# Optimization experiments

Measured on AMD Instinct MI355X. Metric: run time of the kernel, lower is better.

## Reference

```python
import jax, jax.numpy as jnp
import numpy as np

HIDDEN = 4096
NUM_HEADS = 32
GROUP_NUM = 8
HEAD_DIM = HIDDEN // NUM_HEADS


def setup_inputs() -> dict:
    key = jax.random.key(0)
    ks = jax.random.split(key, 9)
    s = 0.02
    kv_dim = GROUP_NUM * HEAD_DIM
    return {
        "hidden_state": jax.random.normal(ks[0], (1, 2048, HIDDEN), dtype=jnp.float32),
        "wq": jax.random.normal(ks[1], (HIDDEN, HIDDEN), dtype=jnp.float32) * s,
        "bq": jnp.zeros((HIDDEN,), dtype=jnp.float32),
        "wk": jax.random.normal(ks[2], (HIDDEN, kv_dim), dtype=jnp.float32) * s,
        "bk": jnp.zeros((kv_dim,), dtype=jnp.float32),
        "wv": jax.random.normal(ks[3], (HIDDEN, kv_dim), dtype=jnp.float32) * s,
        "bv": jnp.zeros((kv_dim,), dtype=jnp.float32),
        "wo": jax.random.normal(ks[4], (HIDDEN, HIDDEN), dtype=jnp.float32) * s,
        "bo": jnp.zeros((HIDDEN,), dtype=jnp.float32),
    }


def reference(hidden_state, wq, bq, wk, bk, wv, bv, wo, bo):
    B, S, _ = hidden_state.shape
    q = hidden_state @ wq + bq                      # [B,S,H*D]
    k = hidden_state @ wk + bk                      # [B,S,G*D]
    v = hidden_state @ wv + bv                      # [B,S,G*D]

    q = q.reshape(B, S, NUM_HEADS, HEAD_DIM).transpose(0, 2, 1, 3)   # [B,H,S,D]
    k = k.reshape(B, S, GROUP_NUM, HEAD_DIM).transpose(0, 2, 1, 3)   # [B,G,S,D]
    v = v.reshape(B, S, GROUP_NUM, HEAD_DIM).transpose(0, 2, 1, 3)
    # broadcast KV groups to all heads (repeat each group heads_per_group times)
    rep = NUM_HEADS // GROUP_NUM
    k = jnp.repeat(k, rep, axis=1)                  # [B,H,S,D]
    v = jnp.repeat(v, rep, axis=1)

    scale = 1.0 / jnp.sqrt(jnp.float32(HEAD_DIM))
    scores = jnp.einsum("bhqd,bhkd->bhqk", q, k) * scale  # [B,H,S,S]
    probs = jax.nn.softmax(scores, axis=-1)
    out = jnp.einsum("bhqk,bhkd->bhqd", probs, v)         # [B,H,S,D]
    # faithful to original: transpose(-1,-2) then view (NOT a standard head merge)
    out = jnp.swapaxes(out, -1, -2).reshape(B, -1, HEAD_DIM * NUM_HEADS)  # [B,S,H*D]
    return out @ wo + bo
```

## Files before the change

### kernel.cpp

```cpp
#include <hip/hip_runtime.h>
#include <stdint.h>

#define HIDDEN 4096
#define SEQ    2048
#define NHEADS 32
#define HDIM   128
#define KVDIM  1024

typedef __attribute__((ext_vector_type(8))) short short8;
typedef __attribute__((ext_vector_type(4))) unsigned short ushort4v;
typedef __attribute__((ext_vector_type(4))) float f32x4;
typedef __attribute__((ext_vector_type(16))) float f32x16;
typedef __attribute__((ext_vector_type(4))) float float4v;
typedef __attribute__((ext_vector_type(4))) int int4v;

__device__ __forceinline__ unsigned short f2bf(float f) {
    union { float f; unsigned u; } v; v.f = f;
    unsigned r = v.u + 0x7FFFu + ((v.u >> 16) & 1u);
    return (unsigned short)(r >> 16);
}

__device__ __forceinline__ float fexp2(float x) {
#if __has_builtin(__builtin_amdgcn_exp2f)
    return __builtin_amdgcn_exp2f(x);
#else
    return exp2f(x);
#endif
}

__device__ __forceinline__ void store_elem(unsigned short* p, float v) { *p = f2bf(v); }
__device__ __forceinline__ void store_elem(float* p, float v) { *p = v; }

__global__ void cast_bf16_kernel(const float* __restrict__ in,
                                 unsigned short* __restrict__ out, int n4) {
    int i = blockIdx.x * blockDim.x + threadIdx.x;
    if (i >= n4) return;
    float4v v = *(const float4v*)(in + (size_t)i * 4);
    ushort4v o;
    o.x = f2bf(v.x); o.y = f2bf(v.y); o.z = f2bf(v.z); o.w = f2bf(v.w);
    *(ushort4v*)(out + (size_t)i * 4) = o;
}

__global__ void transpose_cast_all_kernel(const float* __restrict__ wq,
                                          const float* __restrict__ wk,
                                          const float* __restrict__ wv,
                                          const float* __restrict__ wo,
                                          unsigned short* __restrict__ wqkvt,
                                          unsigned short* __restrict__ wot) {
    __shared__ float tile[64][65];
    int cx = blockIdx.x;
    const float* src; unsigned short* dst; int C; int cxl;
    if (cx < 64)      { src = wq; dst = wqkvt; C = HIDDEN; cxl = cx; }
    else if (cx < 80) { src = wk; dst = wqkvt + (size_t)4096 * HIDDEN; C = KVDIM; cxl = cx - 64; }
    else if (cx < 96) { src = wv; dst = wqkvt + (size_t)5120 * HIDDEN; C = KVDIM; cxl = cx - 80; }
    else              { src = wo; dst = wot;   C = HIDDEN; cxl = cx - 96; }
    const int R = HIDDEN;
    int r0 = blockIdx.y << 6, c0 = cxl << 6;
    int t = threadIdx.x;
    int lr = t >> 4, lc = (t & 15) << 2;
#pragma unroll
    for (int i = 0; i < 4; i++) {
        int r = lr + i * 16;
        float4v v = *(const float4v*)(src + (size_t)(r0 + r) * C + c0 + lc);
        tile[r][lc] = v.x; tile[r][lc + 1] = v.y;
        tile[r][lc + 2] = v.z; tile[r][lc + 3] = v.w;
    }
    __syncthreads();
#pragma unroll
    for (int i = 0; i < 4; i++) {
        int c = lr + i * 16;
        ushort4v o;
        o.x = f2bf(tile[lc][c]);     o.y = f2bf(tile[lc + 1][c]);
        o.z = f2bf(tile[lc + 2][c]); o.w = f2bf(tile[lc + 3][c]);
        *(ushort4v*)(dst + (size_t)(c0 + c) * R + r0 + lc) = o;
    }
}

__device__ __forceinline__ void gload_lds16(const void* g, void* l) {
    __builtin_amdgcn_global_load_lds(
        (const __attribute__((address_space(1))) void*)g,
        (__attribute__((address_space(3))) void*)l, 16, 0, 0);
}

template <typename OT>
__global__ __launch_bounds__(256, 2)
void gemm_bf16_kernel(const unsigned short* __restrict__ A,
                      const unsigned short* __restrict__ Bt,
                      const float* __restrict__ bias,
                      OT* __restrict__ C,
                      int M, int N, int K, float oscale) {
    __shared__ __align__(16) unsigned short As[128 * 32];
    __shared__ __align__(16) unsigned short Bs[128 * 32];
    int t = threadIdx.x;
    int w = t >> 6, l = t & 63;
    int wr = w >> 1, wc = w & 1;
    int fr = l & 15, fq = l >> 4;
    int mbase = blockIdx.y << 7, nbase = blockIdx.x << 7;

    const unsigned short* Ap = A + (size_t)(mbase + w * 16 + (l >> 2)) * K + ((l & 3) << 3);
    const unsigned short* Bp = Bt + (size_t)(nbase + w * 16 + (l >> 2)) * K + ((l & 3) << 3);
    unsigned short* AsW = As + w * 512;
    unsigned short* BsW = Bs + w * 512;
    const size_t rowK64 = (size_t)64 * K;

    f32x4 acc[4][4];
    f32x4 z = {0.f, 0.f, 0.f, 0.f};
#pragma unroll
    for (int m = 0; m < 4; m++)
#pragma unroll
        for (int n = 0; n < 4; n++) acc[m][n] = z;

    for (int kb = 0; kb < K; kb += 32) {
        __syncthreads();
        gload_lds16(Ap + kb,          AsW);
        gload_lds16(Ap + kb + rowK64, AsW + 2048);
        gload_lds16(Bp + kb,          BsW);
        gload_lds16(Bp + kb + rowK64, BsW + 2048);
        __syncthreads();
        short8 a[4], b[4];
#pragma unroll
        for (int m = 0; m < 4; m++)
            a[m] = *(const short8*)(As + ((wr * 64 + m * 16 + fr) * 32 + fq * 8));
#pragma unroll
        for (int n = 0; n < 4; n++)
            b[n] = *(const short8*)(Bs + ((wc * 64 + n * 16 + fr) * 32 + fq * 8));
#pragma unroll
        for (int m = 0; m < 4; m++)
#pragma unroll
            for (int n = 0; n < 4; n++)
                acc[m][n] = __builtin_amdgcn_mfma_f32_16x16x32_bf16(a[m], b[n], acc[m][n], 0, 0, 0);
    }

#pragma unroll
    for (int n = 0; n < 4; n++) {
        int col = nbase + wc * 64 + n * 16 + fr;
        float bv = bias[col];
#pragma unroll
        for (int m = 0; m < 4; m++) {
            int row = mbase + wr * 64 + m * 16 + fq * 4;
            OT* cp = C + (size_t)row * N + col;
#pragma unroll
            for (int r = 0; r < 4; r++)
                store_elem(cp + (size_t)r * N, (acc[m][n][r] + bv) * oscale);
        }
    }
}

__global__ __launch_bounds__(256, 2)
void qkv_gemm_kernel(const unsigned short* __restrict__ A,
                     const unsigned short* __restrict__ Bt,
                     const float* __restrict__ bq,
                     const float* __restrict__ bk,
                     const float* __restrict__ bv,
                     unsigned short* __restrict__ Qo,
                     unsigned short* __restrict__ Ko,
                     unsigned short* __restrict__ Vto,
                     float qscale) {
    const int K = HIDDEN;
    __shared__ __align__(16) unsigned short As[128 * 32];
    __shared__ __align__(16) unsigned short Bs[128 * 32];
    int t = threadIdx.x;
    int w = t >> 6, l = t & 63;
    int wr = w >> 1, wc = w & 1;
    int fr = l & 15, fq = l >> 4;
    int mbase = blockIdx.y << 7, nbase = blockIdx.x << 7;

    const unsigned short* Ap = A + (size_t)(mbase + w * 16 + (l >> 2)) * K + ((l & 3) << 3);
    const unsigned short* Bp = Bt + (size_t)(nbase + w * 16 + (l >> 2)) * K + ((l & 3) << 3);
    unsigned short* AsW = As + w * 512;
    unsigned short* BsW = Bs + w * 512;
    const size_t rowK64 = (size_t)64 * K;

    f32x4 acc[4][4];
    f32x4 z = {0.f, 0.f, 0.f, 0.f};
#pragma unroll
    for (int m = 0; m < 4; m++)
#pragma unroll
        for (int n = 0; n < 4; n++) acc[m][n] = z;

    for (int kb = 0; kb < K; kb += 32) {
        __syncthreads();
        gload_lds16(Ap + kb,          AsW);
        gload_lds16(Ap + kb + rowK64, AsW + 2048);
        gload_lds16(Bp + kb,          BsW);
        gload_lds16(Bp + kb + rowK64, BsW + 2048);
        __syncthreads();
        short8 a[4], b[4];
#pragma unroll
        for (int m = 0; m < 4; m++)
            a[m] = *(const short8*)(As + ((wr * 64 + m * 16 + fr) * 32 + fq * 8));
#pragma unroll
        for (int n = 0; n < 4; n++)
            b[n] = *(const short8*)(Bs + ((wc * 64 + n * 16 + fr) * 32 + fq * 8));
#pragma unroll
        for (int m = 0; m < 4; m++)
#pragma unroll
            for (int n = 0; n < 4; n++)
                acc[m][n] = __builtin_amdgcn_mfma_f32_16x16x32_bf16(a[m], b[n], acc[m][n], 0, 0, 0);
    }

    if (nbase < 4096) {
#pragma unroll
        for (int n = 0; n < 4; n++) {
            int col = nbase + wc * 64 + n * 16 + fr;
            float bb = bq[col];
#pragma unroll
            for (int m = 0; m < 4; m++) {
                int row = mbase + wr * 64 + m * 16 + fq * 4;
                unsigned short* cp = Qo + (size_t)row * HIDDEN + col;
#pragma unroll
                for (int r = 0; r < 4; r++)
                    cp[(size_t)r * HIDDEN] = f2bf((acc[m][n][r] + bb) * qscale);
            }
        }
    } else if (nbase < 5120) {
#pragma unroll
        for (int n = 0; n < 4; n++) {
            int col = nbase - 4096 + wc * 64 + n * 16 + fr;
            float bb = bk[col];
#pragma unroll
            for (int m = 0; m < 4; m++) {
                int row = mbase + wr * 64 + m * 16 + fq * 4;
                unsigned short* cp = Ko + (size_t)row * KVDIM + col;
#pragma unroll
                for (int r = 0; r < 4; r++)
                    cp[(size_t)r * KVDIM] = f2bf(acc[m][n][r] + bb);
            }
        }
    } else {
#pragma unroll
        for (int n = 0; n < 4; n++) {
            int colv = nbase - 5120 + wc * 64 + n * 16 + fr;
            float bb = bv[colv];
#pragma unroll
            for (int m = 0; m < 4; m++) {
                int row = mbase + wr * 64 + m * 16 + fq * 4;
                ushort4v o;
                o.x = f2bf(acc[m][n][0] + bb);
                o.y = f2bf(acc[m][n][1] + bb);
                o.z = f2bf(acc[m][n][2] + bb);
                o.w = f2bf(acc[m][n][3] + bb);
                *(ushort4v*)(Vto + (size_t)colv * SEQ + row) = o;
            }
        }
    }
}

#define SWZ(off, row) ((off) ^ (((row) & 7) << 4))
__global__ __launch_bounds__(256, 2)
void attn_kernel(const unsigned short* __restrict__ Q,
                 const unsigned short* __restrict__ Kc,
                 const unsigned short* __restrict__ Vt,
                 unsigned short* __restrict__ Mg) {
    __shared__ __align__(16) char Kb[2][64 * 256];
    __shared__ __align__(16) char Vb[2][128 * 128];
    int qb = blockIdx.x, head = blockIdx.y, g = head >> 2;
    int t = threadIdx.x, w = t >> 6, l = t & 63;
    int lq = l & 31, lh = l >> 5;

    short8 qf[8];
    {
        const unsigned short* qp =
            Q + (size_t)(qb * 128 + w * 32 + lq) * HIDDEN + head * HDIM + lh * 8;
#pragma unroll
        for (int kk = 0; kk < 8; kk++) qf[kk] = *(const short8*)(qp + kk * 16);
    }

    f32x16 accO[4];
#pragma unroll
    for (int n = 0; n < 4; n++)
#pragma unroll
        for (int r = 0; r < 16; r++) accO[n][r] = 0.f;
    float Lrun = 0.f;

    int krow = t >> 2; int kcb = (t & 3) * 64;
    int vrow = t >> 1; int vcb = (t & 1) * 64;
    const unsigned short* ksrc = Kc + (size_t)krow * KVDIM + g * HDIM + (t & 3) * 32;
    const unsigned short* vsrc = Vt + (size_t)(g * HDIM + vrow) * SEQ + (t & 1) * 32;
    int kwb = krow * 256 + kcb;
    int vwb = vrow * 128 + vcb;

    const int NT = SEQ / 64;
    short8 kreg[4], vreg[4];
#pragma unroll
    for (int j = 0; j < 4; j++) kreg[j] = *(const short8*)(ksrc + j * 8);
#pragma unroll
    for (int j = 0; j < 4; j++) vreg[j] = *(const short8*)(vsrc + j * 8);
#pragma unroll
    for (int j = 0; j < 4; j++) *(short8*)(Kb[0] + SWZ(kwb + j * 16, krow)) = kreg[j];
#pragma unroll
    for (int j = 0; j < 4; j++) *(short8*)(Vb[0] + SWZ(vwb + j * 16, vrow)) = vreg[j];
#pragma unroll
    for (int j = 0; j < 4; j++) kreg[j] = *(const short8*)(ksrc + (size_t)64 * KVDIM + j * 8);
#pragma unroll
    for (int j = 0; j < 4; j++) vreg[j] = *(const short8*)(vsrc + 64 + j * 8);

    for (int tl = 0; tl < NT; tl++) {
        int b = tl & 1;
        __syncthreads();
        if (tl + 1 < NT) {
#pragma unroll
            for (int j = 0; j < 4; j++) *(short8*)(Kb[b ^ 1] + SWZ(kwb + j * 16, krow)) = kreg[j];
#pragma unroll
            for (int j = 0; j < 4; j++) *(short8*)(Vb[b ^ 1] + SWZ(vwb + j * 16, vrow)) = vreg[j];
            if (tl + 2 < NT) {
                const unsigned short* ks = ksrc + (size_t)(tl + 2) * 64 * KVDIM;
                const unsigned short* vs = vsrc + (tl + 2) * 64;
#pragma unroll
                for (int j = 0; j < 4; j++) kreg[j] = *(const short8*)(ks + j * 8);
#pragma unroll
                for (int j = 0; j < 4; j++) vreg[j] = *(const short8*)(vs + j * 8);
            }
        }
        const char* kb = Kb[b];
        const char* vb = Vb[b];

        f32x16 s0, s1;
#pragma unroll
        for (int r = 0; r < 16; r++) { s0[r] = 0.f; s1[r] = 0.f; }
#pragma unroll
        for (int kk = 0; kk < 8; kk++) {
            int cb = kk * 32 + lh * 16;
            short8 kf0 = *(const short8*)(kb + SWZ(lq * 256 + cb, lq));
            short8 kf1 = *(const short8*)(kb + SWZ((lq + 32) * 256 + cb, lq));
            s0 = __builtin_amdgcn_mfma_f32_32x32x16_bf16(kf0, qf[kk], s0, 0, 0, 0);
            s1 = __builtin_amdgcn_mfma_f32_32x32x16_bf16(kf1, qf[kk], s1, 0, 0, 0);
        }

        float sum = 0.f;
#pragma unroll
        for (int r = 0; r < 16; r++) { s0[r] = fexp2(s0[r]); sum += s0[r]; }
#pragma unroll
        for (int r = 0; r < 16; r++) { s1[r] = fexp2(s1[r]); sum += s1[r]; }
        sum += __shfl_xor(sum, 32);
        Lrun += sum;

        int W0[8], W1[8];
#pragma unroll
        for (int i = 0; i < 8; i++)
            W0[i] = (int)((unsigned)f2bf(s0[2 * i]) | ((unsigned)f2bf(s0[2 * i + 1]) << 16));
#pragma unroll
        for (int i = 0; i < 8; i++)
            W1[i] = (int)((unsigned)f2bf(s1[2 * i]) | ((unsigned)f2bf(s1[2 * i + 1]) << 16));

        short8 pa[4];
#pragma unroll
        for (int kkp = 0; kkp < 4; kkp++) {
            int k4 = (kkp & 1) * 4;
            int o0 = (kkp < 2) ? W0[k4 + 0] : W1[k4 + 0];
            int o1 = (kkp < 2) ? W0[k4 + 1] : W1[k4 + 1];
            int o2 = (kkp < 2) ? W0[k4 + 2] : W1[k4 + 2];
            int o3 = (kkp < 2) ? W0[k4 + 3] : W1[k4 + 3];
            int Za = lh ? o0 : o2;
            int Zb = lh ? o1 : o3;
            int Xa = __shfl_xor(Za, 32);
            int Xb = __shfl_xor(Zb, 32);
            int4v pw;
            pw.x = lh ? Xa : o0;
            pw.y = lh ? Xb : o1;
            pw.z = lh ? o2 : Xa;
            pw.w = lh ? o3 : Xb;
            pa[kkp] = *(short8*)&pw;
        }

#pragma unroll
        for (int n = 0; n < 4; n++) {
            int row = n * 32 + lq;
#pragma unroll
            for (int kkp = 0; kkp < 4; kkp++) {
                short8 vf = *(const short8*)(vb + SWZ(row * 128 + kkp * 32 + lh * 16, lq));
                accO[n] = __builtin_amdgcn_mfma_f32_32x32x16_bf16(pa[kkp], vf, accO[n], 0, 0, 0);
            }
        }
    }

    float rl[16];
#pragma unroll
    for (int r = 0; r < 16; r++)
        rl[r] = 1.0f / __shfl(Lrun, (r & 3) + 8 * (r >> 2) + 4 * lh);
#pragma unroll
    for (int n = 0; n < 4; n++) {
        int d = n * 32 + lq;
        int mrow = head * 64 + (d >> 1);
#pragma unroll
        for (int g2 = 0; g2 < 4; g2++) {
            int mcol = (d & 1) * SEQ + qb * 128 + w * 32 + 8 * g2 + 4 * lh;
            ushort4v o;
            o.x = f2bf(accO[n][g2 * 4 + 0] * rl[g2 * 4 + 0]);
            o.y = f2bf(accO[n][g2 * 4 + 1] * rl[g2 * 4 + 1]);
            o.z = f2bf(accO[n][g2 * 4 + 2] * rl[g2 * 4 + 2]);
            o.w = f2bf(accO[n][g2 * 4 + 3] * rl[g2 * 4 + 3]);
            *(ushort4v*)(Mg + (size_t)mrow * HIDDEN + mcol) = o;
        }
    }
}

extern "C" void kernel_launch(void* const* d_in, const int* in_sizes, int n_in,
                              void* d_out, int out_size, void* d_ws, size_t ws_size,
                              hipStream_t stream) {
    const float* x  = (const float*)d_in[0];
    const float* wq = (const float*)d_in[1];
    const float* bq = (const float*)d_in[2];
    const float* wk = (const float*)d_in[3];
    const float* bk = (const float*)d_in[4];
    const float* wv = (const float*)d_in[5];
    const float* bv = (const float*)d_in[6];
    const float* wo = (const float*)d_in[7];
    const float* bo = (const float*)d_in[8];

    char* base = (char*)d_ws;
    unsigned short* xb     = (unsigned short*)(base + 0);
    unsigned short* wqkvt  = (unsigned short*)(base + 16777216);
    unsigned short* wot    = (unsigned short*)(base + 67108864);
    unsigned short* qbuf   = (unsigned short*)(base + 100663296);
    unsigned short* kbuf   = (unsigned short*)(base + 117440512);
    unsigned short* vtbuf  = (unsigned short*)(base + 121634816);
    unsigned short* merged = (unsigned short*)(base + 125829120);

    const float QSCALE = 0.08838834764831845f * 1.4426950408889634f;

    cast_bf16_kernel<<<(SEQ * HIDDEN / 4 + 255) / 256, 256, 0, stream>>>(x, xb, SEQ * HIDDEN / 4);
    transpose_cast_all_kernel<<<dim3(160, 64), 256, 0, stream>>>(wq, wk, wv, wo, wqkvt, wot);
    qkv_gemm_kernel<<<dim3(6144 / 128, SEQ / 128), 256, 0, stream>>>(
        xb, wqkvt, bq, bk, bv, qbuf, kbuf, vtbuf, QSCALE);
    attn_kernel<<<dim3(SEQ / 128, NHEADS), 256, 0, stream>>>(qbuf, kbuf, vtbuf, merged);
    gemm_bf16_kernel<<<dim3(HIDDEN / 128, SEQ / 128), 256, 0, stream>>>(
        merged, wot, bo, (float*)d_out, SEQ, HIDDEN, HIDDEN, 1.0f);
}
```

Measured before the change: 341.9 us.

## Rewrite GEMMs with 128x256 tiles, triple-buffered async LDS pipeline and swizzles

Replaces the two 128x128, 256-thread GEMM kernels with one templated 512-thread kernel. It uses a 128x256 tile with BK=64 and a three-stage LDS ring fed by global_load_lds, with vmcnt waits so loads for tile t+2 overlap compute. It also XOR-swizzles LDS to avoid bank conflicts, remaps workgroups across XCDs for better L2 locality, and raises MFMA priority with setprio. The cost is 144KB of LDS per block and one block per CU, so occupancy drops and latency hiding relies on the pipeline.

```diff
diff --git a/kernel.cpp b/kernel.cpp
--- a/kernel.cpp
+++ b/kernel.cpp
@@ -27,9 +27,6 @@
     return exp2f(x);
 #endif
 }
-
-__device__ __forceinline__ void store_elem(unsigned short* p, float v) { *p = f2bf(v); }
-__device__ __forceinline__ void store_elem(float* p, float v) { *p = v; }
 
 __global__ void cast_bf16_kernel(const float* __restrict__ in,
                                  unsigned short* __restrict__ out, int n4) {
@@ -82,26 +79,58 @@
         (__attribute__((address_space(3))) void*)l, 16, 0, 0);
 }
 
-template <typename OT>
-__global__ __launch_bounds__(256, 2)
-void gemm_bf16_kernel(const unsigned short* __restrict__ A,
-                      const unsigned short* __restrict__ Bt,
-                      const float* __restrict__ bias,
-                      OT* __restrict__ C,
-                      int M, int N, int K, float oscale) {
-    __shared__ __align__(16) unsigned short As[128 * 32];
-    __shared__ __align__(16) unsigned short Bs[128 * 32];
+template <int MODE>
+__global__ __launch_bounds__(512, 1)
+void gemm8_kernel(const unsigned short* __restrict__ A,
+                  const unsigned short* __restrict__ Bt,
+                  const float* __restrict__ b0,
+                  const float* __restrict__ b1,
+                  const float* __restrict__ b2,
+                  unsigned short* __restrict__ Qo,
+                  unsigned short* __restrict__ Ko,
+                  unsigned short* __restrict__ Vto,
+                  float* __restrict__ Of,
+                  float qscale) {
+    const int K = HIDDEN;
+    __shared__ __align__(16) char lds[3 * 49152];
+
     int t = threadIdx.x;
     int w = t >> 6, l = t & 63;
-    int wr = w >> 1, wc = w & 1;
     int fr = l & 15, fq = l >> 4;
-    int mbase = blockIdx.y << 7, nbase = blockIdx.x << 7;
-
-    const unsigned short* Ap = A + (size_t)(mbase + w * 16 + (l >> 2)) * K + ((l & 3) << 3);
-    const unsigned short* Bp = Bt + (size_t)(nbase + w * 16 + (l >> 2)) * K + ((l & 3) << 3);
-    unsigned short* AsW = As + w * 512;
-    unsigned short* BsW = Bs + w * 512;
-    const size_t rowK64 = (size_t)64 * K;
+    int wm = w >> 2, wn = w & 3;
+
+    int nwg = gridDim.x * gridDim.y;
+    int orig = blockIdx.y * gridDim.x + blockIdx.x;
+    int cpx = nwg >> 3;
+    int swz = (orig & 7) * cpx + (orig >> 3);
+    int bx = swz % gridDim.x, by = swz / gridDim.x;
+    int mbase = by * 128, nbase = bx * 256;
+
+    int rA = t >> 3;
+    int lch = (t & 7) ^ (rA & 7);
+    const unsigned short* pA0 = A + (size_t)(mbase + rA) * K + lch * 8;
+    const unsigned short* pA1 = pA0 + (size_t)64 * K;
+    const unsigned short* pB0 = Bt + (size_t)(nbase + rA) * K + lch * 8;
+    const unsigned short* pB1 = pB0 + (size_t)64 * K;
+    const unsigned short* pB2 = pB0 + (size_t)128 * K;
+    const unsigned short* pB3 = pB0 + (size_t)192 * K;
+    int wo16 = w * 1024;
+
+    int offA[4][2], offB[4][2];
+#pragma unroll
+    for (int m = 0; m < 4; m++) {
+        int row = wm * 64 + m * 16 + fr;
+#pragma unroll
+        for (int kk = 0; kk < 2; kk++)
+            offA[m][kk] = row * 128 + (((kk << 2) + fq) ^ (row & 7)) * 16;
+    }
+#pragma unroll
+    for (int n = 0; n < 4; n++) {
+        int row = wn * 64 + n * 16 + fr;
+#pragma unroll
+        for (int kk = 0; kk < 2; kk++)
+            offB[n][kk] = 16384 + row * 128 + (((kk << 2) + fq) ^ (row & 7)) * 16;
+    }
 
     f32x4 acc[4][4];
     f32x4 z = {0.f, 0.f, 0.f, 0.f};
@@ -110,137 +139,111 @@
 #pragma unroll
         for (int n = 0; n < 4; n++) acc[m][n] = z;
 
-    for (int kb = 0; kb < K; kb += 32) {
-        __syncthreads();
-        gload_lds16(Ap + kb,          AsW);
-        gload_lds16(Ap + kb + rowK64, AsW + 2048);
-        gload_lds16(Bp + kb,          BsW);
-        gload_lds16(Bp + kb + rowK64, BsW + 2048);
-        __syncthreads();
-        short8 a[4], b[4];
-#pragma unroll
-        for (int m = 0; m < 4; m++)
-            a[m] = *(const short8*)(As + ((wr * 64 + m * 16 + fr) * 32 + fq * 8));
-#pragma unroll
-        for (int n = 0; n < 4; n++)
-            b[n] = *(const short8*)(Bs + ((wc * 64 + n * 16 + fr) * 32 + fq * 8));
-#pragma unroll
-        for (int m = 0; m < 4; m++)
-#pragma unroll
-            for (int n = 0; n < 4; n++)
-                acc[m][n] = __builtin_amdgcn_mfma_f32_16x16x32_bf16(a[m], b[n], acc[m][n], 0, 0, 0);
-    }
-
-#pragma unroll
-    for (int n = 0; n < 4; n++) {
-        int col = nbase + wc * 64 + n * 16 + fr;
-        float bv = bias[col];
-#pragma unroll
-        for (int m = 0; m < 4; m++) {
-            int row = mbase + wr * 64 + m * 16 + fq * 4;
-            OT* cp = C + (size_t)row * N + col;
-#pragma unroll
-            for (int r = 0; r < 4; r++)
-                store_elem(cp + (size_t)r * N, (acc[m][n][r] + bv) * oscale);
-        }
-    }
-}
-
-__global__ __launch_bounds__(256, 2)
-void qkv_gemm_kernel(const unsigned short* __restrict__ A,
-                     const unsigned short* __restrict__ Bt,
-                     const float* __restrict__ bq,
-                     const float* __restrict__ bk,
-                     const float* __restrict__ bv,
-                     unsigned short* __restrict__ Qo,
-                     unsigned short* __restrict__ Ko,
-                     unsigned short* __restrict__ Vto,
-                     float qscale) {
-    const int K = HIDDEN;
-    __shared__ __align__(16) unsigned short As[128 * 32];
-    __shared__ __align__(16) unsigned short Bs[128 * 32];
-    int t = threadIdx.x;
-    int w = t >> 6, l = t & 63;
-    int wr = w >> 1, wc = w & 1;
-    int fr = l & 15, fq = l >> 4;
-    int mbase = blockIdx.y << 7, nbase = blockIdx.x << 7;
-
-    const unsigned short* Ap = A + (size_t)(mbase + w * 16 + (l >> 2)) * K + ((l & 3) << 3);
-    const unsigned short* Bp = Bt + (size_t)(nbase + w * 16 + (l >> 2)) * K + ((l & 3) << 3);
-    unsigned short* AsW = As + w * 512;
-    unsigned short* BsW = Bs + w * 512;
-    const size_t rowK64 = (size_t)64 * K;
-
-    f32x4 acc[4][4];
-    f32x4 z = {0.f, 0.f, 0.f, 0.f};
-#pragma unroll
-    for (int m = 0; m < 4; m++)
-#pragma unroll
-        for (int n = 0; n < 4; n++) acc[m][n] = z;
-
-    for (int kb = 0; kb < K; kb += 32) {
-        __syncthreads();
-        gload_lds16(Ap + kb,          AsW);
-        gload_lds16(Ap + kb + rowK64, AsW + 2048);
-        gload_lds16(Bp + kb,          BsW);
-        gload_lds16(Bp + kb + rowK64, BsW + 2048);
-        __syncthreads();
-        short8 a[4], b[4];
-#pragma unroll
-        for (int m = 0; m < 4; m++)
-            a[m] = *(const short8*)(As + ((wr * 64 + m * 16 + fr) * 32 + fq * 8));
-#pragma unroll
-        for (int n = 0; n < 4; n++)
-            b[n] = *(const short8*)(Bs + ((wc * 64 + n * 16 + fr) * 32 + fq * 8));
-#pragma unroll
-        for (int m = 0; m < 4; m++)
-#pragma unroll
-            for (int n = 0; n < 4; n++)
-                acc[m][n] = __builtin_amdgcn_mfma_f32_16x16x32_bf16(a[m], b[n], acc[m][n], 0, 0, 0);
-    }
-
-    if (nbase < 4096) {
+    const int NT = K / 64;
+
+#define STAGE6(bufbase, ts)                                            \
+    {                                                                  \
+        size_t ko = (size_t)(ts) * 64;                                 \
+        char* lb = lds + (bufbase);                                    \
+        gload_lds16(pA0 + ko, lb + wo16);                              \
+        gload_lds16(pA1 + ko, lb + 8192 + wo16);                       \
+        gload_lds16(pB0 + ko, lb + 16384 + wo16);                      \
+        gload_lds16(pB1 + ko, lb + 24576 + wo16);                      \
+        gload_lds16(pB2 + ko, lb + 32768 + wo16);                      \
+        gload_lds16(pB3 + ko, lb + 40960 + wo16);                      \
+    }
+
+    STAGE6(0, 0);
+    STAGE6(49152, 1);
+
+    int cb = 0;
+    for (int tt = 0; tt < NT; ++tt) {
+        if (tt + 1 < NT) asm volatile("s_waitcnt vmcnt(6)" ::: "memory");
+        else             asm volatile("s_waitcnt vmcnt(0)" ::: "memory");
+        __builtin_amdgcn_s_barrier();
+        __builtin_amdgcn_sched_barrier(0);
+        if (tt + 2 < NT) {
+            int sb = (cb == 0) ? 2 : cb - 1;
+            STAGE6(sb * 49152, tt + 2);
+        }
+        const char* base = lds + cb * 49152;
+#pragma unroll
+        for (int kk = 0; kk < 2; kk++) {
+            short8 af[4], bf[4];
+#pragma unroll
+            for (int m = 0; m < 4; m++) af[m] = *(const short8*)(base + offA[m][kk]);
+#pragma unroll
+            for (int n = 0; n < 4; n++) bf[n] = *(const short8*)(base + offB[n][kk]);
+            __builtin_amdgcn_s_setprio(1);
+#pragma unroll
+            for (int m = 0; m < 4; m++)
+#pragma unroll
+                for (int n = 0; n < 4; n++)
+                    acc[m][n] = __builtin_amdgcn_mfma_f32_16x16x32_bf16(af[m], bf[n], acc[m][n], 0, 0, 0);
+            __builtin_amdgcn_s_setprio(0);
+        }
+        cb = (cb == 2) ? 0 : cb + 1;
+    }
+#undef STAGE6
+
+    if (MODE == 1) {
+        if (nbase < 4096) {
+#pragma unroll
+            for (int n = 0; n < 4; n++) {
+                int col = nbase + wn * 64 + n * 16 + fr;
+                float bb = b0[col];
+#pragma unroll
+                for (int m = 0; m < 4; m++) {
+                    int row = mbase + wm * 64 + m * 16 + fq * 4;
+                    unsigned short* cp = Qo + (size_t)row * HIDDEN + col;
+#pragma unroll
+                    for (int r = 0; r < 4; r++)
+                        cp[(size_t)r * HIDDEN] = f2bf((acc[m][n][r] + bb) * qscale);
+                }
+            }
+        } else if (nbase < 5120) {
+#pragma unroll
+            for (int n = 0; n < 4; n++) {
+                int col = nbase - 4096 + wn * 64 + n * 16 + fr;
+                float bb = b1[col];
+#pragma unroll
+                for (int m = 0; m < 4; m++) {
+                    int row = mbase + wm * 64 + m * 16 + fq * 4;
+                    unsigned short* cp = Ko + (size_t)row * KVDIM + col;
+#pragma unroll
+                    for (int r = 0; r < 4; r++)
+                        cp[(size_t)r * KVDIM] = f2bf(acc[m][n][r] + bb);
+                }
+            }
+        } else {
+#pragma unroll
+            for (int n = 0; n < 4; n++) {
+                int col = nbase - 5120 + wn * 64 + n * 16 + fr;
+                float bb = b2[col];
+#pragma unroll
+                for (int m = 0; m < 4; m++) {
+                    int row = mbase + wm * 64 + m * 16 + fq * 4;
+                    ushort4v o;
+                    o.x = f2bf(acc[m][n][0] + bb);
+                    o.y = f2bf(acc[m][n][1] + bb);
+                    o.z = f2bf(acc[m][n][2] + bb);
+                    o.w = f2bf(acc[m][n][3] + bb);
+                    *(ushort4v*)(Vto + (size_t)col * SEQ + row) = o;
+                }
+            }
+        }
+    } else {
 #pragma unroll
         for (int n = 0; n < 4; n++) {
-            int col = nbase + wc * 64 + n * 16 + fr;
-            float bb = bq[col];
+            int col = nbase + wn * 64 + n * 16 + fr;
+            float bb = b0[col];
 #pragma unroll
             for (int m = 0; m < 4; m++) {
-                int row = mbase + wr * 64 + m * 16 + fq * 4;
-                unsigned short* cp = Qo + (size_t)row * HIDDEN + col;
+                int row = mbase + wm * 64 + m * 16 + fq * 4;
+                float* cp = Of + (size_t)row * HIDDEN + col;
 #pragma unroll
                 for (int r = 0; r < 4; r++)
-                    cp[(size_t)r * HIDDEN] = f2bf((acc[m][n][r] + bb) * qscale);
-            }
-        }
-    } else if (nbase < 5120) {
-#pragma unroll
-        for (int n = 0; n < 4; n++) {
-            int col = nbase - 4096 + wc * 64 + n * 16 + fr;
-            float bb = bk[col];
-#pragma unroll
-            for (int m = 0; m < 4; m++) {
-                int row = mbase + wr * 64 + m * 16 + fq * 4;
-                unsigned short* cp = Ko + (size_t)row * KVDIM + col;
-#pragma unroll
-                for (int r = 0; r < 4; r++)
-                    cp[(size_t)r * KVDIM] = f2bf(acc[m][n][r] + bb);
-            }
-        }
-    } else {
-#pragma unroll
-        for (int n = 0; n < 4; n++) {
-            int colv = nbase - 5120 + wc * 64 + n * 16 + fr;
-            float bb = bv[colv];
-#pragma unroll
-            for (int m = 0; m < 4; m++) {
-                int row = mbase + wr * 64 + m * 16 + fq * 4;
-                ushort4v o;
-                o.x = f2bf(acc[m][n][0] + bb);
-                o.y = f2bf(acc[m][n][1] + bb);
-                o.z = f2bf(acc[m][n][2] + bb);
-                o.w = f2bf(acc[m][n][3] + bb);
-                *(ushort4v*)(Vto + (size_t)colv * SEQ + row) = o;
+                    cp[(size_t)r * HIDDEN] = acc[m][n][r] + bb;
             }
         }
     }
@@ -320,9 +323,9 @@
         for (int r = 0; r < 16; r++) { s0[r] = 0.f; s1[r] = 0.f; }
 #pragma unroll
         for (int kk = 0; kk < 8; kk++) {
-            int cb = kk * 32 + lh * 16;
-            short8 kf0 = *(const short8*)(kb + SWZ(lq * 256 + cb, lq));
-            short8 kf1 = *(const short8*)(kb + SWZ((lq + 32) * 256 + cb, lq));
+            int cb2 = kk * 32 + lh * 16;
+            short8 kf0 = *(const short8*)(kb + SWZ(lq * 256 + cb2, lq));
+            short8 kf1 = *(const short8*)(kb + SWZ((lq + 32) * 256 + cb2, lq));
             s0 = __builtin_amdgcn_mfma_f32_32x32x16_bf16(kf0, qf[kk], s0, 0, 0, 0);
             s1 = __builtin_amdgcn_mfma_f32_32x32x16_bf16(kf1, qf[kk], s1, 0, 0, 0);
         }
@@ -421,9 +424,9 @@
 
     cast_bf16_kernel<<<(SEQ * HIDDEN / 4 + 255) / 256, 256, 0, stream>>>(x, xb, SEQ * HIDDEN / 4);
     transpose_cast_all_kernel<<<dim3(160, 64), 256, 0, stream>>>(wq, wk, wv, wo, wqkvt, wot);
-    qkv_gemm_kernel<<<dim3(6144 / 128, SEQ / 128), 256, 0, stream>>>(
-        xb, wqkvt, bq, bk, bv, qbuf, kbuf, vtbuf, QSCALE);
+    gemm8_kernel<1><<<dim3(6144 / 256, SEQ / 128), 512, 0, stream>>>(
+        xb, wqkvt, bq, bk, bv, qbuf, kbuf, vtbuf, nullptr, QSCALE);
     attn_kernel<<<dim3(SEQ / 128, NHEADS), 256, 0, stream>>>(qbuf, kbuf, vtbuf, merged);
-    gemm_bf16_kernel<<<dim3(HIDDEN / 128, SEQ / 128), 256, 0, stream>>>(
-        merged, wot, bo, (float*)d_out, SEQ, HIDDEN, HIDDEN, 1.0f);
-}
+    gemm8_kernel<2><<<dim3(HIDDEN / 256, SEQ / 128), 512, 0, stream>>>(
+        merged, wot, bo, nullptr, nullptr, nullptr, nullptr, nullptr, (float*)d_out, 1.0f);
+}
```

After: 328.8 us. -3.8%, faster.
